# Performance work log

Hardware: AMD Instinct MI355X
Metric: run time of the kernel (lower is better)

Reference implementation:

```python
import jax, jax.numpy as jnp
import numpy as np


def _segment_sum(x):
    # x: (..., T). Returns (..., T, T) with [i, j] = sum_{j < k <= i} x[k] for i >= j, else -inf.
    T = x.shape[-1]
    lower = jnp.tril(jnp.ones((T, T), dtype=bool), -1)
    xx = jnp.where(lower, x[..., :, None], 0.0)  # [..., i, j] = x[..., i] for i > j
    seg = jnp.cumsum(xx, axis=-2)
    keep = jnp.tril(jnp.ones((T, T), dtype=bool), 0)
    return jnp.where(keep, seg, -jnp.inf)


def _ssd(x, dt, A, B, C, chunk_len, D):
    # x: (b,s,H,dh)  dt: (b,s,H)  A: (H,)  B,C: (b,s,H,N)
    b, s, H, dh = x.shape
    N = B.shape[-1]
    c = s // chunk_len  # seq_len multiple of chunk_len -> pad_size == 0
    D_res = D[..., None] * x
    x = x * dt[..., None]
    Adt = A.astype(x.dtype) * dt  # (b,s,H)
    xc = x.reshape(b, c, chunk_len, H, dh)
    Ac = Adt.reshape(b, c, chunk_len, H).transpose(0, 3, 1, 2)  # (b,H,c,L)
    Bc = B.reshape(b, c, chunk_len, H, N)
    Cc = C.reshape(b, c, chunk_len, H, N)
    A_cumsum = jnp.cumsum(Ac, axis=-1)  # (b,H,c,L)
    Lmat = jnp.exp(_segment_sum(Ac))  # (b,H,c,L,L)
    # intra-chunk (diagonal) term
    Gm = jnp.einsum('bclhn,bcshn->bclsh', Cc, Bc)
    M = Gm * Lmat.transpose(0, 2, 3, 4, 1)  # (b,c,L,L,H)
    Y_diag = jnp.einsum('bclsh,bcshd->bclhd', M, xc)
    # chunk states
    decay_states = jnp.exp(A_cumsum[..., -1:] - A_cumsum)  # (b,H,c,L)
    B_decay = Bc * decay_states.transpose(0, 2, 3, 1)[..., None]
    states = jnp.einsum('bclhn,bclhd->bchdn', B_decay, xc)  # (b,c,H,dh,N)
    states = jnp.concatenate([jnp.zeros_like(states[:, :1]), states], axis=1)  # (b,c+1,H,dh,N)
    decay_chunk = jnp.exp(_segment_sum(jnp.pad(A_cumsum[..., -1], ((0, 0), (0, 0), (1, 0)))))  # (b,H,c+1,c+1)
    # Faithful to the source module: (decay[...,None,None] * states[:, :, None]).sum(dim=2)
    # sums over the z (row) axis -> equivalent to scaling states by the column sums of decay_chunk.
    col_sum = decay_chunk.sum(axis=2)  # (b,H,c+1)
    new_states = states * col_sum.transpose(0, 2, 1)[..., None, None]  # (b,c+1,H,dh,N)
    states = new_states[:, :-1]  # (b,c,H,dh,N)
    # inter-chunk (off-diagonal) term
    Y_off = jnp.einsum('bclhn,bchdn->bclhd', Cc, states) * jnp.exp(A_cumsum).transpose(0, 2, 3, 1)[..., None]
    return (Y_diag + Y_off).reshape(b, s, H, dh) + D_res


def setup_inputs() -> dict:
    key = jax.random.key(0)
    ks = jax.random.split(key, 6)
    b, s, dm, H, N, G = 2, 2048, 2048, 32, 128, 8
    sc = 0.02
    return {
        'hidden_states': jax.random.normal(ks[0], (b, s, dm), jnp.float32),
        'A_log': jnp.log(jnp.arange(1, H + 1, dtype=jnp.float32)),
        'D': jnp.ones((H,), jnp.float32),
        'W_B': jax.random.normal(ks[1], (dm, G * N), jnp.float32) * sc,
        'b_B': jnp.zeros((G * N,), jnp.float32),
        'W_C': jax.random.normal(ks[2], (dm, G * N), jnp.float32) * sc,
        'b_C': jnp.zeros((G * N,), jnp.float32),
        'W_x': jax.random.normal(ks[3], (dm, dm), jnp.float32) * sc,
        'b_x': jnp.zeros((dm,), jnp.float32),
        'W_dt': jax.random.normal(ks[4], (dm, H), jnp.float32) * sc,
        'b_dt': jnp.zeros((H,), jnp.float32),
        'W_out': jax.random.normal(ks[5], (dm, dm), jnp.float32) * sc,
        'b_out': jnp.zeros((dm,), jnp.float32),
        'chunk_len': 256,
        'd_state': 128,
    }


def reference(hidden_states, A_log, D, W_B, b_B, W_C, b_C, W_x, b_x, W_dt, b_dt, W_out, b_out, chunk_len, d_state):
    b, s, dm = hidden_states.shape
    H = A_log.shape[0]
    G = W_B.shape[1] // d_state
    A = -jnp.exp(A_log)
    Bm = (hidden_states @ W_B + b_B).reshape(b, s, G, d_state)
    Bm = jnp.tile(Bm, (1, 1, H // G, 1))  # torch .repeat tiles groups over heads
    Cm = (hidden_states @ W_C + b_C).reshape(b, s, G, d_state)
    Cm = jnp.tile(Cm, (1, 1, H // G, 1))
    dt = jax.nn.softplus(hidden_states @ W_dt + b_dt)  # (b,s,H)
    x = (hidden_states @ W_x + b_x).reshape(b, s, H, dm // H)
    y = _ssd(x, dt, A, Bm, Cm, chunk_len, D)
    return y.reshape(b, s, dm) @ W_out + b_out
```

## Files before the change

kernel.cpp:

```cpp
#include <hip/hip_runtime.h>

#define S_   2048
#define BB   2
#define MR   4096
#define DM   2048
#define HH   32
#define DH   64
#define GG   8
#define NST  128
#define NC   8
#define LCH  256
#define KD   2048

typedef __attribute__((ext_vector_type(4))) float f32x4;
typedef __attribute__((ext_vector_type(8))) short bf16x8;

__device__ __forceinline__ short f2bf(float f) {
  unsigned u = __builtin_bit_cast(unsigned, f);
  u += 0x7FFFu + ((u >> 16) & 1u);
  return (short)(u >> 16);
}
__device__ __forceinline__ float bf2f(short s) {
  unsigned u = ((unsigned)(unsigned short)s) << 16;
  return __builtin_bit_cast(float, u);
}
__device__ __forceinline__ unsigned pack2(short lo, short hi) {
  return (unsigned)(unsigned short)lo | ((unsigned)(unsigned short)hi << 16);
}

__global__ void k_cast(const float* __restrict__ src, short* __restrict__ dst, int n8) {
  int i = blockIdx.x * 256 + threadIdx.x;
  if (i >= n8) return;
  const float4 a = *(const float4*)(src + (size_t)i * 8);
  const float4 b = *(const float4*)(src + (size_t)i * 8 + 4);
  uint4 o;
  o.x = pack2(f2bf(a.x), f2bf(a.y));
  o.y = pack2(f2bf(a.z), f2bf(a.w));
  o.z = pack2(f2bf(b.x), f2bf(b.y));
  o.w = pack2(f2bf(b.z), f2bf(b.w));
  *(uint4*)(dst + (size_t)i * 8) = o;
}

__global__ __launch_bounds__(256) void k_cast_T(const float* __restrict__ src,
                                                short* __restrict__ dst, int K, int N) {
  __shared__ short t[32][33];
  int bx = blockIdx.x * 32, by = blockIdx.y * 32;
  int tx = threadIdx.x & 31, ty = threadIdx.x >> 5;
  for (int r = ty; r < 32; r += 8)
    t[r][tx] = f2bf(src[(size_t)(by + r) * N + bx + tx]);
  __syncthreads();
  for (int r = ty; r < 32; r += 8)
    dst[(size_t)(bx + r) * K + by + tx] = t[tx][r];
}

template <int OUT_BF16>
__global__ __launch_bounds__(256) void k_gemm(const short* __restrict__ A,
                                              const short* __restrict__ Bt,
                                              const float* __restrict__ bias,
                                              void* __restrict__ out, int M, int N, int K) {
  __shared__ short As[64 * 40];
  __shared__ short Bs[64 * 40];
  const int tid = threadIdx.x;
  const int bm = blockIdx.y * 64, bn = blockIdx.x * 64;
  const int wid = tid >> 6, lane = tid & 63, lg = lane >> 4, lr = lane & 15;
  const int wr = wid >> 1, wc = wid & 1;
  const int arow = tid >> 2, aseg = (tid & 3) * 8;
  const bool bok = (bn + arow) < N;
  const short* Arow = A + (size_t)(bm + arow) * K + aseg;
  const short* Brow = Bt + (size_t)(bn + arow) * K + aseg;
  f32x4 acc[2][2] = {};
  for (int k0 = 0; k0 < K; k0 += 32) {
    uint4 av = *(const uint4*)(Arow + k0);
    uint4 bv;
    if (bok) bv = *(const uint4*)(Brow + k0);
    else     bv = make_uint4(0u, 0u, 0u, 0u);
    __syncthreads();
    *(uint4*)(As + arow * 40 + aseg) = av;
    *(uint4*)(Bs + arow * 40 + aseg) = bv;
    __syncthreads();
    bf16x8 af0 = *(const bf16x8*)(As + (wr * 32 + lr) * 40 + lg * 8);
    bf16x8 af1 = *(const bf16x8*)(As + (wr * 32 + 16 + lr) * 40 + lg * 8);
    bf16x8 bf0 = *(const bf16x8*)(Bs + (wc * 32 + lr) * 40 + lg * 8);
    bf16x8 bf1 = *(const bf16x8*)(Bs + (wc * 32 + 16 + lr) * 40 + lg * 8);
    acc[0][0] = __builtin_amdgcn_mfma_f32_16x16x32_bf16(af0, bf0, acc[0][0], 0, 0, 0);
    acc[0][1] = __builtin_amdgcn_mfma_f32_16x16x32_bf16(af0, bf1, acc[0][1], 0, 0, 0);
    acc[1][0] = __builtin_amdgcn_mfma_f32_16x16x32_bf16(af1, bf0, acc[1][0], 0, 0, 0);
    acc[1][1] = __builtin_amdgcn_mfma_f32_16x16x32_bf16(af1, bf1, acc[1][1], 0, 0, 0);
  }
  for (int mi = 0; mi < 2; ++mi)
    for (int ni = 0; ni < 2; ++ni) {
      int col = bn + wc * 32 + ni * 16 + lr;
      if (col >= N) continue;
      float bv = bias[col];
      int row0 = bm + wr * 32 + mi * 16 + lg * 4;
      for (int r = 0; r < 4; ++r) {
        float v = acc[mi][ni][r] + bv;
        if (OUT_BF16) ((short*)out)[(size_t)(row0 + r) * N + col] = f2bf(v);
        else          ((float*)out)[(size_t)(row0 + r) * N + col] = v;
      }
    }
}

__global__ void k_dt(const float* __restrict__ dtraw, const float* __restrict__ A_log,
                     float* __restrict__ dtsp, float* __restrict__ adt, int n) {
  int i = blockIdx.x * 256 + threadIdx.x;
  if (i >= n) return;
  int h = i & (HH - 1);
  float z = dtraw[i];
  float sp = (z > 20.f) ? z : log1pf(expf(z));
  dtsp[i] = sp;
  adt[i] = -expf(A_log[h]) * sp;
}

__global__ void k_xdt(const float* __restrict__ xraw, const float* __restrict__ dtsp,
                      short* __restrict__ xbf, int n4) {
  int i = blockIdx.x * 256 + threadIdx.x;
  if (i >= n4) return;
  size_t e = (size_t)i * 4;
  int row = (int)(e >> 11);
  int col = (int)(e & (DM - 1));
  int h = col >> 6;
  float dt = dtsp[row * HH + h];
  float4 v = *(const float4*)(xraw + e);
  uint2 o;
  o.x = pack2(f2bf(v.x * dt), f2bf(v.y * dt));
  o.y = pack2(f2bf(v.z * dt), f2bf(v.w * dt));
  *(uint2*)(xbf + e) = o;
}

__global__ __launch_bounds__(256) void k_scan(const float* __restrict__ adt,
                                              float* __restrict__ acs,
                                              float* __restrict__ asum) {
  int blk = blockIdx.x;
  int h = blk & 31, ci = (blk >> 5) & 7, b = blk >> 8;
  int l = threadIdx.x;
  __shared__ float sc[256];
  sc[l] = adt[(size_t)(b * S_ + ci * LCH + l) * HH + h];
  __syncthreads();
  for (int o = 1; o < 256; o <<= 1) {
    float t = (l >= o) ? sc[l - o] : 0.f;
    float own = sc[l];
    __syncthreads();
    sc[l] = own + t;
    __syncthreads();
  }
  float r = sc[l];
  acs[((size_t)((b * HH + h) * NC + ci)) * LCH + l] = r;
  if (l == 255) asum[(b * HH + h) * NC + ci] = r;
}

__global__ void k_colsum(const float* __restrict__ asum, float* __restrict__ csum) {
  int t = threadIdx.x;
  if (t >= BB * HH) return;
  float av[NC];
  for (int k = 0; k < NC; ++k) av[k] = asum[t * NC + k];
  for (int z = 0; z < NC; ++z) {
    float run = 0.f, acc = 1.f;
    for (int j = z; j < NC; ++j) { run += av[j]; acc += __expf(run); }
    csum[t * NC + z] = acc;
  }
}

__global__ __launch_bounds__(256) void k_states(const short* __restrict__ Bbf,
                                                const short* __restrict__ xdt,
                                                const float* __restrict__ acs,
                                                const float* __restrict__ asum,
                                                short* __restrict__ state) {
  int blk = blockIdx.x;
  int h = blk & 31, ci = (blk >> 5) & 7, b = blk >> 8;
  int g = h & 7;
  int tid = threadIdx.x, wid = tid >> 6, lane = tid & 63, lg = lane >> 4, lr = lane & 15;
  __shared__ float dsh[256];
  __shared__ short Bt[128 * 40];
  __shared__ short Xt[64 * 40];
  const float* acs_p = acs + ((size_t)((b * HH + h) * NC + ci)) * LCH;
  float last = asum[(b * HH + h) * NC + ci];
  dsh[tid] = __expf(last - acs_p[tid]);
  const short* Bbase = Bbf + ((size_t)(b * S_ + ci * LCH) * GG + g) * NST;
  const short* Xbase = xdt + (size_t)(b * S_ + ci * LCH) * DM + h * DH;
  const int lrow = tid >> 3, nseg = (tid & 7) * 16, dseg = (tid & 7) * 8;
  f32x4 acc[2][4] = {};
  for (int l0 = 0; l0 < LCH; l0 += 32) {
    uint4 b0 = *(const uint4*)(Bbase + (size_t)(l0 + lrow) * (GG * NST) + nseg);
    uint4 b1 = *(const uint4*)(Bbase + (size_t)(l0 + lrow) * (GG * NST) + nseg + 8);
    uint4 xv = *(const uint4*)(Xbase + (size_t)(l0 + lrow) * DM + dseg);
    __syncthreads();
    float dly = dsh[l0 + lrow];
    const short* bp0 = (const short*)&b0;
    for (int e = 0; e < 8; ++e) Bt[(nseg + e) * 40 + lrow] = f2bf(bf2f(bp0[e]) * dly);
    const short* bp1 = (const short*)&b1;
    for (int e = 0; e < 8; ++e) Bt[(nseg + 8 + e) * 40 + lrow] = f2bf(bf2f(bp1[e]) * dly);
    const short* xp = (const short*)&xv;
    for (int e = 0; e < 8; ++e) Xt[(dseg + e) * 40 + lrow] = xp[e];
    __syncthreads();
    bf16x8 afr[2], bfr[4];
    for (int mi = 0; mi < 2; ++mi)
      afr[mi] = *(const bf16x8*)(Bt + (wid * 32 + mi * 16 + lr) * 40 + lg * 8);
    for (int ni = 0; ni < 4; ++ni)
      bfr[ni] = *(const bf16x8*)(Xt + (ni * 16 + lr) * 40 + lg * 8);
    for (int mi = 0; mi < 2; ++mi)
      for (int ni = 0; ni < 4; ++ni)
        acc[mi][ni] = __builtin_amdgcn_mfma_f32_16x16x32_bf16(afr[mi], bfr[ni], acc[mi][ni], 0, 0, 0);
  }
  short* sp = state + (size_t)blk * DH * NST;
  for (int mi = 0; mi < 2; ++mi)
    for (int ni = 0; ni < 4; ++ni)
      for (int r = 0; r < 4; ++r) {
        int n = wid * 32 + mi * 16 + lg * 4 + r;
        int d = ni * 16 + lr;
        sp[d * NST + n] = f2bf(acc[mi][ni][r]);
      }
}

__global__ __launch_bounds__(256) void k_y(const short* __restrict__ Cbf,
                                           const short* __restrict__ Bbf,
                                           const short* __restrict__ xdt,
                                           const float* __restrict__ xraw,
                                           const float* __restrict__ acs,
                                           const float* __restrict__ csum,
                                           const short* __restrict__ state,
                                           const float* __restrict__ Dv,
                                           short* __restrict__ Ybuf) {
  int blk = blockIdx.x;
  int h = blk & 31, ci = (blk >> 5) & 7, b = blk >> 8;
  int g = h & 7;
  int tid = threadIdx.x, wid = tid >> 6, lane = tid & 63, lg = lane >> 4, lr = lane & 15;
  __shared__ float ash[256];
  __shared__ short Xt[64 * 264];
  __shared__ short Mld[4][64 * 40];
  const float* acs_p = acs + ((size_t)((b * HH + h) * NC + ci)) * LCH;
  ash[tid] = acs_p[tid];
  float cs = csum[(b * HH + h) * NC + ci];
  const short* Xbase = xdt + (size_t)(b * S_ + ci * LCH) * DM + h * DH;
  {
    const short* xr = Xbase + (size_t)tid * DM;
    for (int d0 = 0; d0 < DH; d0 += 8) {
      uint4 v = *(const uint4*)(xr + d0);
      const short* vp = (const short*)&v;
      for (int e = 0; e < 8; ++e) Xt[(d0 + e) * 264 + tid] = vp[e];
    }
  }
  __syncthreads();
  f32x4 acc[4][4] = {};
  const short* Crow0 = Cbf + ((size_t)(b * S_ + ci * LCH) * GG + g) * NST;
  if (ci > 0) {
    const short* sp = state + (size_t)((b * NC + ci - 1) * HH + h) * DH * NST;
    for (int n0 = 0; n0 < NST; n0 += 32) {
      bf16x8 afr[4], bfr[4];
      for (int mi = 0; mi < 4; ++mi)
        afr[mi] = *(const bf16x8*)(Crow0 + (size_t)(wid * 64 + mi * 16 + lr) * (GG * NST) + n0 + lg * 8);
      for (int ni = 0; ni < 4; ++ni)
        bfr[ni] = *(const bf16x8*)(sp + (ni * 16 + lr) * NST + n0 + lg * 8);
      for (int mi = 0; mi < 4; ++mi)
        for (int ni = 0; ni < 4; ++ni)
          acc[mi][ni] = __builtin_amdgcn_mfma_f32_16x16x32_bf16(afr[mi], bfr[ni], acc[mi][ni], 0, 0, 0);
    }
    for (int mi = 0; mi < 4; ++mi)
      for (int r = 0; r < 4; ++r) {
        int i = wid * 64 + mi * 16 + lg * 4 + r;
        float f = __expf(ash[i]) * cs;
        for (int ni = 0; ni < 4; ++ni) acc[mi][ni][r] *= f;
      }
  }
  short* Ml = &Mld[wid][0];
  int jtmax = (wid * 64 + 63) >> 5;
  for (int jt = 0; jt <= jtmax; ++jt) {
    f32x4 gacc[4][2] = {};
    for (int n0 = 0; n0 < NST; n0 += 32) {
      bf16x8 afr[4], bfr[2];
      for (int mi = 0; mi < 4; ++mi)
        afr[mi] = *(const bf16x8*)(Crow0 + (size_t)(wid * 64 + mi * 16 + lr) * (GG * NST) + n0 + lg * 8);
      for (int nj = 0; nj < 2; ++nj) {
        int j = jt * 32 + nj * 16 + lr;
        bfr[nj] = *(const bf16x8*)(Bbf + ((size_t)(b * S_ + ci * LCH + j) * GG + g) * NST + n0 + lg * 8);
      }
      for (int mi = 0; mi < 4; ++mi)
        for (int nj = 0; nj < 2; ++nj)
          gacc[mi][nj] = __builtin_amdgcn_mfma_f32_16x16x32_bf16(afr[mi], bfr[nj], gacc[mi][nj], 0, 0, 0);
    }
    for (int mi = 0; mi < 4; ++mi)
      for (int nj = 0; nj < 2; ++nj)
        for (int r = 0; r < 4; ++r) {
          int i = wid * 64 + mi * 16 + lg * 4 + r;
          int jc = jt * 32 + nj * 16 + lr;
          float v = 0.f;
          if (jc <= i) v = gacc[mi][nj][r] * __expf(ash[i] - ash[jc]);
          Ml[(mi * 16 + lg * 4 + r) * 40 + nj * 16 + lr] = f2bf(v);
        }
    bf16x8 mfr[4], xfr[4];
    for (int mi = 0; mi < 4; ++mi) mfr[mi] = *(const bf16x8*)(Ml + (mi * 16 + lr) * 40 + lg * 8);
    for (int ni = 0; ni < 4; ++ni) xfr[ni] = *(const bf16x8*)(Xt + (ni * 16 + lr) * 264 + jt * 32 + lg * 8);
    for (int mi = 0; mi < 4; ++mi)
      for (int ni = 0; ni < 4; ++ni)
        acc[mi][ni] = __builtin_amdgcn_mfma_f32_16x16x32_bf16(mfr[mi], xfr[ni], acc[mi][ni], 0, 0, 0);
  }
  float Dh = Dv[h];
  const float* xr0 = xraw + (size_t)(b * S_ + ci * LCH) * DM + h * DH;
  short* yb = Ybuf + (size_t)(b * S_ + ci * LCH) * DM + h * DH;
  for (int mi = 0; mi < 4; ++mi)
    for (int r = 0; r < 4; ++r) {
      int i = wid * 64 + mi * 16 + lg * 4 + r;
      for (int ni = 0; ni < 4; ++ni) {
        int d = ni * 16 + lr;
        float v = acc[mi][ni][r] + Dh * xr0[(size_t)i * DM + d];
        yb[(size_t)i * DM + d] = f2bf(v);
      }
    }
}

extern "C" void kernel_launch(void* const* d_in, const int* in_sizes, int n_in,
                              void* d_out, int out_size, void* d_ws, size_t ws_size,
                              hipStream_t stream) {
  const float* hs    = (const float*)d_in[0];
  const float* A_log = (const float*)d_in[1];
  const float* Dv    = (const float*)d_in[2];
  const float* W_B   = (const float*)d_in[3];
  const float* b_B   = (const float*)d_in[4];
  const float* W_C   = (const float*)d_in[5];
  const float* b_C   = (const float*)d_in[6];
  const float* W_x   = (const float*)d_in[7];
  const float* b_x   = (const float*)d_in[8];
  const float* W_dt  = (const float*)d_in[9];
  const float* b_dt  = (const float*)d_in[10];
  const float* W_out = (const float*)d_in[11];
  const float* b_out = (const float*)d_in[12];

  char* w = (char*)d_ws;
  size_t off = 0;
  auto alloc = [&](size_t bytes) -> char* {
    char* p = w + off;
    off += (bytes + 255) & ~(size_t)255;
    return p;
  };
  short* hs_bf = (short*)alloc((size_t)MR * DM * 2);
  short* WxT   = (short*)alloc((size_t)DM * DM * 2);
  short* WBT   = (short*)alloc((size_t)1024 * DM * 2);
  short* WCT   = (short*)alloc((size_t)1024 * DM * 2);
  short* WdtT  = (short*)alloc((size_t)32 * DM * 2);
  short* WoutT = (short*)alloc((size_t)DM * DM * 2);
  float* xraw  = (float*)alloc((size_t)MR * DM * 4);
  short* Bbf   = (short*)alloc((size_t)MR * 1024 * 2);
  short* Cbf   = (short*)alloc((size_t)MR * 1024 * 2);
  float* dtraw = (float*)alloc((size_t)MR * HH * 4);
  float* dtsp  = (float*)alloc((size_t)MR * HH * 4);
  float* adt   = (float*)alloc((size_t)MR * HH * 4);
  float* acs   = (float*)alloc((size_t)BB * HH * NC * LCH * 4);
  float* asum  = (float*)alloc((size_t)BB * HH * NC * 4);
  float* csum  = (float*)alloc((size_t)BB * HH * NC * 4);
  short* state = (short*)alloc((size_t)BB * NC * HH * DH * NST * 2);
  short* xdtbf = (short*)alloc((size_t)MR * DM * 2);
  short* Ybuf  = (short*)alloc((size_t)MR * DM * 2);
  (void)ws_size; (void)in_sizes; (void)n_in; (void)out_size;

  k_cast<<<(MR * DM / 8 + 255) / 256, 256, 0, stream>>>(hs, hs_bf, MR * DM / 8);
  k_cast_T<<<dim3(DM / 32, DM / 32), 256, 0, stream>>>(W_x, WxT, DM, DM);
  k_cast_T<<<dim3(1024 / 32, DM / 32), 256, 0, stream>>>(W_B, WBT, DM, 1024);
  k_cast_T<<<dim3(1024 / 32, DM / 32), 256, 0, stream>>>(W_C, WCT, DM, 1024);
  k_cast_T<<<dim3(1, DM / 32), 256, 0, stream>>>(W_dt, WdtT, DM, 32);
  k_cast_T<<<dim3(DM / 32, DM / 32), 256, 0, stream>>>(W_out, WoutT, DM, DM);

  k_gemm<0><<<dim3(1, MR / 64), 256, 0, stream>>>(hs_bf, WdtT, b_dt, dtraw, MR, 32, KD);
  k_gemm<0><<<dim3(DM / 64, MR / 64), 256, 0, stream>>>(hs_bf, WxT, b_x, xraw, MR, DM, KD);
  k_gemm<1><<<dim3(1024 / 64, MR / 64), 256, 0, stream>>>(hs_bf, WBT, b_B, Bbf, MR, 1024, KD);
  k_gemm<1><<<dim3(1024 / 64, MR / 64), 256, 0, stream>>>(hs_bf, WCT, b_C, Cbf, MR, 1024, KD);

  k_dt<<<(MR * HH + 255) / 256, 256, 0, stream>>>(dtraw, A_log, dtsp, adt, MR * HH);
  k_xdt<<<(MR * DM / 4 + 255) / 256, 256, 0, stream>>>(xraw, dtsp, xdtbf, MR * DM / 4);
  k_scan<<<BB * HH * NC, 256, 0, stream>>>(adt, acs, asum);
  k_colsum<<<1, 64, 0, stream>>>(asum, csum);

  k_states<<<BB * NC * HH, 256, 0, stream>>>(Bbf, xdtbf, acs, asum, state);
  k_y<<<BB * NC * HH, 256, 0, stream>>>(Cbf, Bbf, xdtbf, xraw, acs, csum, state, Dv, Ybuf);

  k_gemm<0><<<dim3(DM / 64, MR / 64), 256, 0, stream>>>(Ybuf, WoutT, b_out, (float*)d_out, MR, DM, KD);
}
```

Baseline: 525.8 us.

## Add 128x128-tile bf16 MFMA GEMM with direct global-to-LDS loads for large projections

Adds a new GEMM kernel where each block computes a 128x128 output tile and each wave holds a 4x4 grid of 16x16 MFMA accumulators. The previous 64x64 kernel used a 2x2 grid per wave. Operand tiles move straight from global memory into LDS through the global_load_lds builtin instead of passing through registers. The x, B, C and output projections switch to this kernel, which should raise arithmetic intensity and cut global traffic and per-tile overhead. The trade-offs are an unpadded LDS layout that may cause bank conflicts on fragment reads, no double buffering, higher register use, and fewer blocks per launch.

```diff
diff --git a/kernel.cpp b/kernel.cpp
--- a/kernel.cpp
+++ b/kernel.cpp
@@ -14,6 +14,9 @@
 
 typedef __attribute__((ext_vector_type(4))) float f32x4;
 typedef __attribute__((ext_vector_type(8))) short bf16x8;
+
+typedef __attribute__((address_space(1))) const void gvoid;
+typedef __attribute__((address_space(3))) void lvoid;
 
 __device__ __forceinline__ short f2bf(float f) {
   unsigned u = __builtin_bit_cast(unsigned, f);
@@ -93,6 +96,55 @@
       if (col >= N) continue;
       float bv = bias[col];
       int row0 = bm + wr * 32 + mi * 16 + lg * 4;
+      for (int r = 0; r < 4; ++r) {
+        float v = acc[mi][ni][r] + bv;
+        if (OUT_BF16) ((short*)out)[(size_t)(row0 + r) * N + col] = f2bf(v);
+        else          ((float*)out)[(size_t)(row0 + r) * N + col] = v;
+      }
+    }
+}
+
+template <int OUT_BF16>
+__global__ __launch_bounds__(256) void k_gemm128(const short* __restrict__ A,
+                                                 const short* __restrict__ Bt,
+                                                 const float* __restrict__ bias,
+                                                 void* __restrict__ out,
+                                                 int M, int N, int K) {
+  __shared__ short As[128 * 32];
+  __shared__ short Bs[128 * 32];
+  const int tid = threadIdx.x;
+  const int bm = blockIdx.y * 128, bn = blockIdx.x * 128;
+  const int wid = tid >> 6, lane = tid & 63, lg = lane >> 4, lr = lane & 15;
+  const int wr = wid >> 1, wc = wid & 1;
+  const int srow = tid >> 2, skseg = (tid & 3) * 8;
+  const short* gA0 = A + (size_t)(bm + srow) * K + skseg;
+  const short* gA1 = A + (size_t)(bm + 64 + srow) * K + skseg;
+  const short* gB0 = Bt + (size_t)(bn + srow) * K + skseg;
+  const short* gB1 = Bt + (size_t)(bn + 64 + srow) * K + skseg;
+  char* lA = (char*)As + wid * 1024;
+  char* lB = (char*)Bs + wid * 1024;
+  f32x4 acc[4][4] = {};
+  for (int k0 = 0; k0 < K; k0 += 32) {
+    __syncthreads();
+    __builtin_amdgcn_global_load_lds((gvoid*)(gA0 + k0), (lvoid*)lA, 16, 0, 0);
+    __builtin_amdgcn_global_load_lds((gvoid*)(gA1 + k0), (lvoid*)(lA + 4096), 16, 0, 0);
+    __builtin_amdgcn_global_load_lds((gvoid*)(gB0 + k0), (lvoid*)lB, 16, 0, 0);
+    __builtin_amdgcn_global_load_lds((gvoid*)(gB1 + k0), (lvoid*)(lB + 4096), 16, 0, 0);
+    __syncthreads();
+    bf16x8 af[4], bfv[4];
+    for (int mi = 0; mi < 4; ++mi)
+      af[mi] = *(const bf16x8*)(As + (wr * 64 + mi * 16 + lr) * 32 + lg * 8);
+    for (int ni = 0; ni < 4; ++ni)
+      bfv[ni] = *(const bf16x8*)(Bs + (wc * 64 + ni * 16 + lr) * 32 + lg * 8);
+    for (int mi = 0; mi < 4; ++mi)
+      for (int ni = 0; ni < 4; ++ni)
+        acc[mi][ni] = __builtin_amdgcn_mfma_f32_16x16x32_bf16(af[mi], bfv[ni], acc[mi][ni], 0, 0, 0);
+  }
+  for (int mi = 0; mi < 4; ++mi)
+    for (int ni = 0; ni < 4; ++ni) {
+      int col = bn + wc * 64 + ni * 16 + lr;
+      float bv = bias[col];
+      int row0 = bm + wr * 64 + mi * 16 + lg * 4;
       for (int r = 0; r < 4; ++r) {
         float v = acc[mi][ni][r] + bv;
         if (OUT_BF16) ((short*)out)[(size_t)(row0 + r) * N + col] = f2bf(v);
@@ -360,9 +412,9 @@
   k_cast_T<<<dim3(DM / 32, DM / 32), 256, 0, stream>>>(W_out, WoutT, DM, DM);
 
   k_gemm<0><<<dim3(1, MR / 64), 256, 0, stream>>>(hs_bf, WdtT, b_dt, dtraw, MR, 32, KD);
-  k_gemm<0><<<dim3(DM / 64, MR / 64), 256, 0, stream>>>(hs_bf, WxT, b_x, xraw, MR, DM, KD);
-  k_gemm<1><<<dim3(1024 / 64, MR / 64), 256, 0, stream>>>(hs_bf, WBT, b_B, Bbf, MR, 1024, KD);
-  k_gemm<1><<<dim3(1024 / 64, MR / 64), 256, 0, stream>>>(hs_bf, WCT, b_C, Cbf, MR, 1024, KD);
+  k_gemm128<0><<<dim3(DM / 128, MR / 128), 256, 0, stream>>>(hs_bf, WxT, b_x, xraw, MR, DM, KD);
+  k_gemm128<1><<<dim3(1024 / 128, MR / 128), 256, 0, stream>>>(hs_bf, WBT, b_B, Bbf, MR, 1024, KD);
+  k_gemm128<1><<<dim3(1024 / 128, MR / 128), 256, 0, stream>>>(hs_bf, WCT, b_C, Cbf, MR, 1024, KD);
 
   k_dt<<<(MR * HH + 255) / 256, 256, 0, stream>>>(dtraw, A_log, dtsp, adt, MR * HH);
   k_xdt<<<(MR * DM / 4 + 255) / 256, 256, 0, stream>>>(xraw, dtsp, xdtbf, MR * DM / 4);
@@ -372,5 +424,5 @@
   k_states<<<BB * NC * HH, 256, 0, stream>>>(Bbf, xdtbf, acs, asum, state);
   k_y<<<BB * NC * HH, 256, 0, stream>>>(Cbf, Bbf, xdtbf, xraw, acs, csum, state, Dv, Ybuf);
 
-  k_gemm<0><<<dim3(DM / 64, MR / 64), 256, 0, stream>>>(Ybuf, WoutT, b_out, (float*)d_out, MR, DM, KD);
-}
+  k_gemm128<0><<<dim3(DM / 128, MR / 128), 256, 0, stream>>>(Ybuf, WoutT, b_out, (float*)d_out, MR, DM, KD);
+}
```

Result: faster. 470.8 us (-10.5%).
